# Optimization experiments

Hardware: AMD Instinct MI355X
Metric: run time of the kernel (lower is better)

The kernel has to match this reference:

```python
import jax, jax.numpy as jnp
import numpy as np

EPS = 1e-10
ENTROPY_COEF = 0.1
COLSUM_COEF = 1.0


def setup_inputs() -> dict:
    key = jax.random.key(0)
    k1, k2, k3 = jax.random.split(key, 3)
    H, T, B, S = 512, 50003, 32, 256
    colsum_threshold = 0.5
    return {
        "text_input": jax.random.randint(k1, (B, S), 0, T, dtype=jnp.int32),
        "init_logits": jnp.zeros((H,), dtype=jnp.float32),
        "transition_logits": jax.random.normal(k2, (H, H), dtype=jnp.float32) * 0.1,
        "emission_logits": jax.random.normal(k3, (H, T), dtype=jnp.float32) * 0.1,
        "colsum_threshold": colsum_threshold,
    }


def reference(text_input, init_logits, transition_logits, emission_logits, colsum_threshold):
    # softmax-normalized HMM parameters
    text_pi = jax.nn.softmax(init_logits, axis=0)              # [H]
    text_A = jax.nn.softmax(transition_logits, axis=1)         # [H,H]
    text_B = jax.nn.softmax(emission_logits, axis=1)           # [H,T]

    log_pi = jnp.log(text_pi + EPS)                            # [H]
    log_A = jnpp = jnp.log(text_A + EPS)                       # [H,H]
    log_B = jnp.log(text_B + EPS)                              # [H,T]

    # gather per-token emission log-probs: [B,S,H]
    log_B_obs = log_B.T[text_input]

    # t = 0
    log_alpha0 = log_pi[None, :] + log_B_obs[:, 0, :]          # [B,H]

    def step(log_alpha, obs_t):
        # logsumexp over source state i: [B,H(i),1] + [1,H(i),H(j)] -> [B,H(j)]
        trans = log_alpha[:, :, None] + log_A[None, :, :]
        new_alpha = jax.nn.logsumexp(trans, axis=1) + obs_t
        return new_alpha, None

    obs_rest = jnp.swapaxes(log_B_obs[:, 1:, :], 0, 1)         # [S-1,B,H]
    log_alpha_final, _ = jax.lax.scan(step, log_alpha0, obs_rest)

    log_likelihood = jax.nn.logsumexp(log_alpha_final, axis=1)  # [B]
    likelihood_loss = -jnp.mean(log_likelihood)

    transition_entropy = -jnp.sum(text_A * jnp.log(text_A + EPS), axis=1)
    transition_entropy_loss = jnp.mean(transition_entropy) * ENTROPY_COEF

    col_sums = jnp.sum(text_A, axis=0)
    colsum_reg = jnp.sum(jax.nn.relu(colsum_threshold - col_sums)) * COLSUM_COEF

    hmm_loss = likelihood_loss + transition_entropy_loss + colsum_reg
    return text_pi, text_A, text_B, hmm_loss
```

## Files before the change

kernel.cpp:

```cpp
#include <hip/hip_runtime.h>
#include <hip/hip_bf16.h>
#include <stdint.h>

#define HH 512
#define BB 32
#define SSEQ 256
#define TVOC 50003
#define EPSF 1e-10f
#define EMSCALE 96.0f
#define TOTLOG 2759.2459164008406f

typedef float f32x4 __attribute__((ext_vector_type(4)));
typedef int v8i __attribute__((ext_vector_type(8)));

__device__ __forceinline__ float wave_max(float v) {
#pragma unroll
  for (int off = 32; off; off >>= 1) v = fmaxf(v, __shfl_xor(v, off));
  return v;
}
__device__ __forceinline__ float wave_sum(float v) {
#pragma unroll
  for (int off = 32; off; off >>= 1) v += __shfl_xor(v, off);
  return v;
}

__global__ __launch_bounds__(512) void init_ws_kernel(float* ws) {
  if (threadIdx.x < 8) ws[threadIdx.x] = 0.0f;
  ws[8 + threadIdx.x] = 0.0f;
}

__global__ __launch_bounds__(512) void softmax_pi_kernel(
    const float* __restrict__ x, float* __restrict__ pi) {
  const int tid = threadIdx.x;
  const int wv = tid >> 6, ln = tid & 63;
  __shared__ float red[8];
  float v = x[tid];
  float m = wave_max(v);
  if (ln == 0) red[wv] = m;
  __syncthreads();
  float M = red[0];
#pragma unroll
  for (int i = 1; i < 8; ++i) M = fmaxf(M, red[i]);
  float e = __expf(v - M);
  float s = wave_sum(e);
  __syncthreads();
  if (ln == 0) red[wv] = s;
  __syncthreads();
  float S = 0.f;
#pragma unroll
  for (int i = 0; i < 8; ++i) S += red[i];
  pi[tid] = e / S;
}

__global__ __launch_bounds__(512) void softmaxA_kernel(
    const float* __restrict__ tl, float* __restrict__ outA,
    float* __restrict__ ws_ent) {
  const int r = blockIdx.x, tid = threadIdx.x;
  const int wv = tid >> 6, ln = tid & 63;
  __shared__ float red[8];
  float v = tl[(size_t)r * HH + tid];
  float m = wave_max(v);
  if (ln == 0) red[wv] = m;
  __syncthreads();
  float M = red[0];
#pragma unroll
  for (int i = 1; i < 8; ++i) M = fmaxf(M, red[i]);
  float e = __expf(v - M);
  float s = wave_sum(e);
  __syncthreads();
  if (ln == 0) red[wv] = s;
  __syncthreads();
  float S = 0.f;
#pragma unroll
  for (int i = 0; i < 8; ++i) S += red[i];
  float p = e / S;
  outA[(size_t)r * HH + tid] = p;
  float ent = -p * __logf(p + EPSF);
  ent = wave_sum(ent);
  __syncthreads();
  if (ln == 0) red[wv] = ent;
  __syncthreads();
  if (tid == 0) {
    float tot = 0.f;
#pragma unroll
    for (int i = 0; i < 8; ++i) tot += red[i];
    atomicAdd(ws_ent, tot);
  }
}

__global__ __launch_bounds__(512) void colsum_partial_kernel(
    const float* __restrict__ outA, float* __restrict__ col) {
  const int j = threadIdx.x;
  const int i0 = blockIdx.x * 64;
  float s = 0.f;
#pragma unroll 4
  for (int i = i0; i < i0 + 64; ++i) s += outA[(size_t)i * HH + j];
  atomicAdd(&col[j], s);
}

__global__ __launch_bounds__(1024) void softmaxB_gather_kernel(
    const float* __restrict__ el, float* __restrict__ outB,
    const int* __restrict__ tok, __hip_bfloat16* __restrict__ ems) {
  const int r = blockIdx.x, tid = threadIdx.x;
  const float* x = el + (size_t)r * TVOC;
  float* yo = outB + (size_t)r * TVOC;
  const int mis = (int)(((16u - ((unsigned)(uintptr_t)x & 15u)) & 15u) >> 2);
  const int body = (TVOC - mis) >> 2;
  const int tailoff = mis + body * 4;

  float m = -1e30f, s = 0.f;
  auto upd = [&m, &s](float v) {
    if (v > m) { s = s * __expf(m - v) + 1.f; m = v; }
    else       { s += __expf(v - m); }
  };
  if (tid < mis) upd(x[tid]);
  const float4* x4 = (const float4*)(x + mis);
  for (int i = tid; i < body; i += 1024) {
    float4 v = x4[i];
    upd(v.x); upd(v.y); upd(v.z); upd(v.w);
  }
  for (int i = tailoff + tid; i < TVOC; i += 1024) upd(x[i]);

#pragma unroll
  for (int off = 32; off; off >>= 1) {
    float om = __shfl_down(m, off), os = __shfl_down(s, off);
    float nm = fmaxf(m, om);
    s = s * __expf(m - nm) + os * __expf(om - nm);
    m = nm;
  }
  __shared__ float sm[16], ssv[16];
  __shared__ float bM, biZ;
  if ((tid & 63) == 0) { sm[tid >> 6] = m; ssv[tid >> 6] = s; }
  __syncthreads();
  if (tid == 0) {
    float M = sm[0], S = ssv[0];
#pragma unroll
    for (int w = 1; w < 16; ++w) {
      float nm = fmaxf(M, sm[w]);
      S = S * __expf(M - nm) + ssv[w] * __expf(sm[w] - nm);
      M = nm;
    }
    bM = M; biZ = 1.f / S;
  }
  __syncthreads();
  const float M = bM, iZ = biZ;
  if (tid < mis) yo[tid] = __expf(x[tid] - M) * iZ;
  float4* y4 = (float4*)(yo + mis);
  for (int i = tid; i < body; i += 1024) {
    float4 v = x4[i];
    float4 o;
    o.x = __expf(v.x - M) * iZ;
    o.y = __expf(v.y - M) * iZ;
    o.z = __expf(v.z - M) * iZ;
    o.w = __expf(v.w - M) * iZ;
    y4[i] = o;
  }
  for (int i = tailoff + tid; i < TVOC; i += 1024)
    yo[i] = __expf(x[i] - M) * iZ;

  const float gs = EMSCALE * iZ;
  for (int idx = tid; idx < BB * SSEQ; idx += 1024) {
    const int sq = idx >> 5, b = idx & 31;
    const int t = tok[b * SSEQ + sq];
    ems[((size_t)sq * HH + r) * BB + b] = __float2bfloat16(__expf(x[t] - M) * gs);
  }
}

__global__ __launch_bounds__(1024) void scan_kernel(
    const float* __restrict__ d_pi, const float* __restrict__ d_A,
    const __hip_bfloat16* __restrict__ ems, float* __restrict__ ws_negll) {
  const int h = blockIdx.x;
  const int tid = threadIdx.x;
  const int lane = tid & 63;
  const int wave = tid >> 6;
  const int l15 = lane & 15;
  const int quad = lane >> 4;

  __shared__ __align__(16) unsigned char alpha[2][16][528];
  __shared__ float wmax[16][17];
  __shared__ float wsum[16][17];
  __shared__ float ls[16];

  const unsigned short* emsu = (const unsigned short*)ems;

  v8i aF[2][4];
#pragma unroll
  for (int n = 0; n < 2; ++n) {
    const int jg = wave * 32 + n * 16 + l15;
#pragma unroll
    for (int c = 0; c < 4; ++c) {
#pragma unroll
      for (int g = 0; g < 8; ++g) {
        const int k0 = c * 128 + quad * 32 + g * 4;
        const float v0 = d_A[(size_t)(k0 + 0) * HH + jg] * 512.0f;
        const float v1 = d_A[(size_t)(k0 + 1) * HH + jg] * 512.0f;
        const float v2 = d_A[(size_t)(k0 + 2) * HH + jg] * 512.0f;
        const float v3 = d_A[(size_t)(k0 + 3) * HH + jg] * 512.0f;
        int wrd = 0;
        wrd = __builtin_amdgcn_cvt_pk_fp8_f32(v0, v1, wrd, false);
        wrd = __builtin_amdgcn_cvt_pk_fp8_f32(v2, v3, wrd, true);
        aF[n][c][g] = wrd;
      }
    }
  }

  {
    const int b = wave;
    const int j0 = lane * 8;
    float vals[8];
    float m = -1e30f;
#pragma unroll
    for (int u = 0; u < 8; ++u) {
      const float e = __bfloat162float(ems[(size_t)(j0 + u) * BB + h * 16 + b]);
      vals[u] = (d_pi[j0 + u] + EPSF) * e;
      m = fmaxf(m, vals[u]);
    }
    m = wave_max(m);
    if (lane == 0) ls[b] = __logf(m);
    const float r = 1.0f / m;
    int lo = 0, hi = 0;
    lo = __builtin_amdgcn_cvt_pk_fp8_f32(vals[0] * r, vals[1] * r, lo, false);
    lo = __builtin_amdgcn_cvt_pk_fp8_f32(vals[2] * r, vals[3] * r, lo, true);
    hi = __builtin_amdgcn_cvt_pk_fp8_f32(vals[4] * r, vals[5] * r, hi, false);
    hi = __builtin_amdgcn_cvt_pk_fp8_f32(vals[6] * r, vals[7] * r, hi, true);
    *(unsigned int*)&alpha[0][b][j0]     = (unsigned)lo;
    *(unsigned int*)&alpha[0][b][j0 + 4] = (unsigned)hi;
  }
  __syncthreads();

  unsigned short evr[2][4];
#pragma unroll
  for (int n = 0; n < 2; ++n)
#pragma unroll
    for (int rg = 0; rg < 4; ++rg) {
      const int j = wave * 32 + n * 16 + quad * 4 + rg;
      evr[n][rg] = emsu[((size_t)1 * HH + j) * BB + h * 16 + l15];
    }

#pragma unroll 1
  for (int t = 1; t < SSEQ; ++t) {
    const int cur = (t - 1) & 1, nxt = t & 1;

    float ev[2][4];
#pragma unroll
    for (int n = 0; n < 2; ++n)
#pragma unroll
      for (int rg = 0; rg < 4; ++rg) {
        const unsigned u = (unsigned)evr[n][rg] << 16;
        ev[n][rg] = __uint_as_float(u);
      }
    const int tp = (t + 1 < SSEQ) ? t + 1 : SSEQ - 1;
#pragma unroll
    for (int n = 0; n < 2; ++n)
#pragma unroll
      for (int rg = 0; rg < 4; ++rg) {
        const int j = wave * 32 + n * 16 + quad * 4 + rg;
        evr[n][rg] = emsu[((size_t)tp * HH + j) * BB + h * 16 + l15];
      }

    f32x4 acc0 = {0.f, 0.f, 0.f, 0.f}, acc1 = {0.f, 0.f, 0.f, 0.f};
#pragma unroll
    for (int c = 0; c < 4; ++c) {
      const unsigned char* ap = &alpha[cur][l15][c * 128 + quad * 32];
      const int4 lo = *(const int4*)ap;
      const int4 hi = *(const int4*)(ap + 16);
      v8i bf;
      bf[0] = lo.x; bf[1] = lo.y; bf[2] = lo.z; bf[3] = lo.w;
      bf[4] = hi.x; bf[5] = hi.y; bf[6] = hi.z; bf[7] = hi.w;
      acc0 = __builtin_amdgcn_mfma_scale_f32_16x16x128_f8f6f4(
          aF[0][c], bf, acc0, 0, 0, 0, 0x7F7F7F7F, 0, 0x7F7F7F7F);
      acc1 = __builtin_amdgcn_mfma_scale_f32_16x16x128_f8f6f4(
          aF[1][c], bf, acc1, 0, 0, 0, 0x7F7F7F7F, 0, 0x7F7F7F7F);
    }

    float y[2][4];
#pragma unroll
    for (int rg = 0; rg < 4; ++rg) {
      y[0][rg] = acc0[rg] * ev[0][rg];
      y[1][rg] = acc1[rg] * ev[1][rg];
    }

    float r = 1.0f;
    if ((t & 15) == 0) {
      float mm = -1e30f;
#pragma unroll
      for (int rg = 0; rg < 4; ++rg)
        mm = fmaxf(mm, fmaxf(y[0][rg], y[1][rg]));
      mm = fmaxf(mm, __shfl_xor(mm, 16));
      mm = fmaxf(mm, __shfl_xor(mm, 32));
      if (lane < 16) wmax[wave][lane] = mm;
      __syncthreads();
      float m = wmax[0][l15];
#pragma unroll
      for (int w = 1; w < 16; ++w) m = fmaxf(m, wmax[w][l15]);
      r = 1.0f / m;
      if (tid < 16) ls[tid] += __logf(m);
    }

#pragma unroll
    for (int n = 0; n < 2; ++n) {
      int d = 0;
      d = __builtin_amdgcn_cvt_pk_fp8_f32(y[n][0] * r, y[n][1] * r, d, false);
      d = __builtin_amdgcn_cvt_pk_fp8_f32(y[n][2] * r, y[n][3] * r, d, true);
      *(unsigned int*)&alpha[nxt][l15][wave * 32 + n * 16 + quad * 4] = (unsigned)d;
    }
    if (t == SSEQ - 1) {
      float s = (y[0][0] + y[0][1] + y[0][2] + y[0][3] +
                 y[1][0] + y[1][1] + y[1][2] + y[1][3]) * r;
      s += __shfl_xor(s, 16);
      s += __shfl_xor(s, 32);
      if (lane < 16) wsum[wave][lane] = s;
    }
    __syncthreads();
  }

  if (wave == 0 && lane < 16) {
    float s = 0.f;
#pragma unroll
    for (int w = 0; w < 16; ++w) s += wsum[w][lane];
    const float LL = __logf(s) + ls[lane] - TOTLOG;
    atomicAdd(ws_negll, -LL * (1.0f / 32.0f));
  }
}

__global__ __launch_bounds__(512) void finalize_kernel(
    const float* __restrict__ ws, const float* __restrict__ col,
    const float* __restrict__ thr, float* __restrict__ out_loss) {
  const int j = threadIdx.x;
  float v = fmaxf(thr[0] - col[j], 0.f);
  v = wave_sum(v);
  __shared__ float red[8];
  if ((j & 63) == 0) red[j >> 6] = v;
  __syncthreads();
  if (j == 0) {
    float creg = 0.f;
#pragma unroll
    for (int i = 0; i < 8; ++i) creg += red[i];
    out_loss[0] = ws[1] + ws[0] * (0.1f / 512.0f) + creg;
  }
}

extern "C" void kernel_launch(void* const* d_in, const int* in_sizes, int n_in,
                              void* d_out, int out_size, void* d_ws, size_t ws_size,
                              hipStream_t stream) {
  const int*   tok    = (const int*)d_in[0];
  const float* initl  = (const float*)d_in[1];
  const float* transl = (const float*)d_in[2];
  const float* eml    = (const float*)d_in[3];
  const float* thr    = (const float*)d_in[4];

  float* out      = (float*)d_out;
  float* out_pi   = out;
  float* out_A    = out + HH;
  float* out_B    = out + HH + (size_t)HH * HH;
  float* out_loss = out + HH + (size_t)HH * HH + (size_t)HH * TVOC;

  float* wsf = (float*)d_ws;
  float* col = wsf + 8;
  __hip_bfloat16* ems = (__hip_bfloat16*)((char*)d_ws + 4096);

  init_ws_kernel<<<1, 512, 0, stream>>>(wsf);
  softmax_pi_kernel<<<1, 512, 0, stream>>>(initl, out_pi);
  softmaxA_kernel<<<512, 512, 0, stream>>>(transl, out_A, wsf + 0);
  colsum_partial_kernel<<<8, 512, 0, stream>>>(out_A, col);
  softmaxB_gather_kernel<<<512, 1024, 0, stream>>>(eml, out_B, tok, ems);
  scan_kernel<<<2, 1024, 0, stream>>>(out_pi, out_A, ems, wsf + 1);
  finalize_kernel<<<1, 512, 0, stream>>>(wsf, col, thr, out_loss);
}
```

Baseline: 596.8 us.

## Halve scan block to 8 waves, repack emission layout for vector loads, split softmax accumulators

The scan kernel now runs 512 threads per block, with each wave computing 64 output states (four MFMA accumulators) instead of 32. This cuts the cost of the per-step block barrier and the cross-wave max reduction. The emission buffer is re-laid out so each lane fetches four consecutive states' bf16 values in one 8-byte load rather than four scalar loads. The loop is also unrolled by two. The softmaxB online max/sum now keeps four independent accumulator chains per thread to break the serial dependency, which costs extra registers and a final merge.

```diff
diff --git a/kernel.cpp b/kernel.cpp
--- a/kernel.cpp
+++ b/kernel.cpp
@@ -108,18 +108,26 @@
   const int body = (TVOC - mis) >> 2;
   const int tailoff = mis + body * 4;
 
-  float m = -1e30f, s = 0.f;
-  auto upd = [&m, &s](float v) {
+  float m0 = -1e30f, s0 = 0.f, m1 = -1e30f, s1 = 0.f;
+  float m2 = -1e30f, s2 = 0.f, m3 = -1e30f, s3 = 0.f;
+  auto upd = [](float& m, float& s, float v) {
     if (v > m) { s = s * __expf(m - v) + 1.f; m = v; }
     else       { s += __expf(v - m); }
   };
-  if (tid < mis) upd(x[tid]);
+  if (tid < mis) upd(m0, s0, x[tid]);
   const float4* x4 = (const float4*)(x + mis);
   for (int i = tid; i < body; i += 1024) {
     float4 v = x4[i];
-    upd(v.x); upd(v.y); upd(v.z); upd(v.w);
-  }
-  for (int i = tailoff + tid; i < TVOC; i += 1024) upd(x[i]);
+    upd(m0, s0, v.x); upd(m1, s1, v.y); upd(m2, s2, v.z); upd(m3, s3, v.w);
+  }
+  for (int i = tailoff + tid; i < TVOC; i += 1024) upd(m0, s0, x[i]);
+  auto mrg = [](float& m, float& s, float om, float os) {
+    float nm = fmaxf(m, om);
+    s = s * __expf(m - nm) + os * __expf(om - nm);
+    m = nm;
+  };
+  mrg(m0, s0, m1, s1); mrg(m2, s2, m3, s3); mrg(m0, s0, m2, s2);
+  float m = m0, s = s0;
 
 #pragma unroll
   for (int off = 32; off; off >>= 1) {
@@ -159,14 +167,16 @@
     yo[i] = __expf(x[i] - M) * iZ;
 
   const float gs = EMSCALE * iZ;
+  const int rg = r >> 2, rl = r & 3;
   for (int idx = tid; idx < BB * SSEQ; idx += 1024) {
     const int sq = idx >> 5, b = idx & 31;
     const int t = tok[b * SSEQ + sq];
-    ems[((size_t)sq * HH + r) * BB + b] = __float2bfloat16(__expf(x[t] - M) * gs);
-  }
-}
-
-__global__ __launch_bounds__(1024) void scan_kernel(
+    ems[((size_t)(sq * 128 + rg) * 32 + b) * 4 + rl] =
+        __float2bfloat16(__expf(x[t] - M) * gs);
+  }
+}
+
+__global__ __launch_bounds__(512, 2) void scan_kernel(
     const float* __restrict__ d_pi, const float* __restrict__ d_A,
     const __hip_bfloat16* __restrict__ ems, float* __restrict__ ws_negll) {
   const int h = blockIdx.x;
@@ -175,18 +185,20 @@
   const int wave = tid >> 6;
   const int l15 = lane & 15;
   const int quad = lane >> 4;
+  const int bG = h * 16 + l15;
 
   __shared__ __align__(16) unsigned char alpha[2][16][528];
-  __shared__ float wmax[16][17];
-  __shared__ float wsum[16][17];
+  __shared__ float wmax[8][17];
+  __shared__ float wsum[8][17];
   __shared__ float ls[16];
 
   const unsigned short* emsu = (const unsigned short*)ems;
-
-  v8i aF[2][4];
-#pragma unroll
-  for (int n = 0; n < 2; ++n) {
-    const int jg = wave * 32 + n * 16 + l15;
+  const uint2* emv = (const uint2*)ems;
+
+  v8i aF[4][4];
+#pragma unroll
+  for (int n = 0; n < 4; ++n) {
+    const int jg = wave * 64 + n * 16 + l15;
 #pragma unroll
     for (int c = 0; c < 4; ++c) {
 #pragma unroll
@@ -204,15 +216,18 @@
     }
   }
 
-  {
-    const int b = wave;
+#pragma unroll
+  for (int it = 0; it < 2; ++it) {
+    const int b = wave * 2 + it;
+    const int bb = h * 16 + b;
     const int j0 = lane * 8;
     float vals[8];
     float m = -1e30f;
 #pragma unroll
     for (int u = 0; u < 8; ++u) {
-      const float e = __bfloat162float(ems[(size_t)(j0 + u) * BB + h * 16 + b]);
-      vals[u] = (d_pi[j0 + u] + EPSF) * e;
+      const int j = j0 + u;
+      const unsigned ew = (unsigned)emsu[((size_t)(j >> 2) * 32 + bb) * 4 + (j & 3)] << 16;
+      vals[u] = (d_pi[j] + EPSF) * __uint_as_float(ew);
       m = fmaxf(m, vals[u]);
     }
     m = wave_max(m);
@@ -228,85 +243,85 @@
   }
   __syncthreads();
 
-  unsigned short evr[2][4];
-#pragma unroll
-  for (int n = 0; n < 2; ++n)
-#pragma unroll
-    for (int rg = 0; rg < 4; ++rg) {
-      const int j = wave * 32 + n * 16 + quad * 4 + rg;
-      evr[n][rg] = emsu[((size_t)1 * HH + j) * BB + h * 16 + l15];
-    }
-
-#pragma unroll 1
+  const uint2* ep = emv + ((size_t)1 * 128 + wave * 16 + quad) * 32 + bG;
+  uint2 evr[4];
+#pragma unroll
+  for (int n = 0; n < 4; ++n) evr[n] = ep[n * 128];
+  ep += 128 * 32;
+
+#pragma unroll 2
   for (int t = 1; t < SSEQ; ++t) {
     const int cur = (t - 1) & 1, nxt = t & 1;
 
-    float ev[2][4];
-#pragma unroll
-    for (int n = 0; n < 2; ++n)
-#pragma unroll
-      for (int rg = 0; rg < 4; ++rg) {
-        const unsigned u = (unsigned)evr[n][rg] << 16;
-        ev[n][rg] = __uint_as_float(u);
-      }
-    const int tp = (t + 1 < SSEQ) ? t + 1 : SSEQ - 1;
-#pragma unroll
-    for (int n = 0; n < 2; ++n)
-#pragma unroll
-      for (int rg = 0; rg < 4; ++rg) {
-        const int j = wave * 32 + n * 16 + quad * 4 + rg;
-        evr[n][rg] = emsu[((size_t)tp * HH + j) * BB + h * 16 + l15];
-      }
+    float ev[4][4];
+#pragma unroll
+    for (int n = 0; n < 4; ++n) {
+      ev[n][0] = __uint_as_float(evr[n].x << 16);
+      ev[n][1] = __uint_as_float(evr[n].x & 0xFFFF0000u);
+      ev[n][2] = __uint_as_float(evr[n].y << 16);
+      ev[n][3] = __uint_as_float(evr[n].y & 0xFFFF0000u);
+    }
+#pragma unroll
+    for (int n = 0; n < 4; ++n) evr[n] = ep[n * 128];
+    if (t <= SSEQ - 3) ep += 128 * 32;
 
     f32x4 acc0 = {0.f, 0.f, 0.f, 0.f}, acc1 = {0.f, 0.f, 0.f, 0.f};
+    f32x4 acc2 = {0.f, 0.f, 0.f, 0.f}, acc3 = {0.f, 0.f, 0.f, 0.f};
 #pragma unroll
     for (int c = 0; c < 4; ++c) {
       const unsigned char* ap = &alpha[cur][l15][c * 128 + quad * 32];
-      const int4 lo = *(const int4*)ap;
-      const int4 hi = *(const int4*)(ap + 16);
       v8i bf;
-      bf[0] = lo.x; bf[1] = lo.y; bf[2] = lo.z; bf[3] = lo.w;
-      bf[4] = hi.x; bf[5] = hi.y; bf[6] = hi.z; bf[7] = hi.w;
+      *(int4*)&bf       = *(const int4*)ap;
+      *(((int4*)&bf)+1) = *(const int4*)(ap + 16);
       acc0 = __builtin_amdgcn_mfma_scale_f32_16x16x128_f8f6f4(
           aF[0][c], bf, acc0, 0, 0, 0, 0x7F7F7F7F, 0, 0x7F7F7F7F);
       acc1 = __builtin_amdgcn_mfma_scale_f32_16x16x128_f8f6f4(
           aF[1][c], bf, acc1, 0, 0, 0, 0x7F7F7F7F, 0, 0x7F7F7F7F);
-    }
-
-    float y[2][4];
+      acc2 = __builtin_amdgcn_mfma_scale_f32_16x16x128_f8f6f4(
+          aF[2][c], bf, acc2, 0, 0, 0, 0x7F7F7F7F, 0, 0x7F7F7F7F);
+      acc3 = __builtin_amdgcn_mfma_scale_f32_16x16x128_f8f6f4(
+          aF[3][c], bf, acc3, 0, 0, 0, 0x7F7F7F7F, 0, 0x7F7F7F7F);
+    }
+
+    float y[4][4];
 #pragma unroll
     for (int rg = 0; rg < 4; ++rg) {
       y[0][rg] = acc0[rg] * ev[0][rg];
       y[1][rg] = acc1[rg] * ev[1][rg];
+      y[2][rg] = acc2[rg] * ev[2][rg];
+      y[3][rg] = acc3[rg] * ev[3][rg];
     }
 
     float r = 1.0f;
     if ((t & 15) == 0) {
       float mm = -1e30f;
 #pragma unroll
-      for (int rg = 0; rg < 4; ++rg)
-        mm = fmaxf(mm, fmaxf(y[0][rg], y[1][rg]));
+      for (int n = 0; n < 4; ++n)
+#pragma unroll
+        for (int rg = 0; rg < 4; ++rg) mm = fmaxf(mm, y[n][rg]);
       mm = fmaxf(mm, __shfl_xor(mm, 16));
       mm = fmaxf(mm, __shfl_xor(mm, 32));
       if (lane < 16) wmax[wave][lane] = mm;
       __syncthreads();
       float m = wmax[0][l15];
 #pragma unroll
-      for (int w = 1; w < 16; ++w) m = fmaxf(m, wmax[w][l15]);
+      for (int w = 1; w < 8; ++w) m = fmaxf(m, wmax[w][l15]);
       r = 1.0f / m;
       if (tid < 16) ls[tid] += __logf(m);
     }
 
 #pragma unroll
-    for (int n = 0; n < 2; ++n) {
+    for (int n = 0; n < 4; ++n) {
       int d = 0;
       d = __builtin_amdgcn_cvt_pk_fp8_f32(y[n][0] * r, y[n][1] * r, d, false);
       d = __builtin_amdgcn_cvt_pk_fp8_f32(y[n][2] * r, y[n][3] * r, d, true);
-      *(unsigned int*)&alpha[nxt][l15][wave * 32 + n * 16 + quad * 4] = (unsigned)d;
+      *(unsigned int*)&alpha[nxt][l15][wave * 64 + n * 16 + quad * 4] = (unsigned)d;
     }
     if (t == SSEQ - 1) {
-      float s = (y[0][0] + y[0][1] + y[0][2] + y[0][3] +
-                 y[1][0] + y[1][1] + y[1][2] + y[1][3]) * r;
+      float s = 0.f;
+#pragma unroll
+      for (int n = 0; n < 4; ++n) s += y[n][0] + y[n][1] + y[n][2] + y[n][3];
+      s *= r;
       s += __shfl_xor(s, 16);
       s += __shfl_xor(s, 32);
       if (lane < 16) wsum[wave][lane] = s;
@@ -317,7 +332,7 @@
   if (wave == 0 && lane < 16) {
     float s = 0.f;
 #pragma unroll
-    for (int w = 0; w < 16; ++w) s += wsum[w][lane];
+    for (int w = 0; w < 8; ++w) s += wsum[w][lane];
     const float LL = __logf(s) + ls[lane] - TOTLOG;
     atomicAdd(ws_negll, -LL * (1.0f / 32.0f));
   }
@@ -364,6 +379,6 @@
   softmaxA_kernel<<<512, 512, 0, stream>>>(transl, out_A, wsf + 0);
   colsum_partial_kernel<<<8, 512, 0, stream>>>(out_A, col);
   softmaxB_gather_kernel<<<512, 1024, 0, stream>>>(eml, out_B, tok, ems);
-  scan_kernel<<<2, 1024, 0, stream>>>(out_pi, out_A, ems, wsf + 1);
+  scan_kernel<<<2, 512, 0, stream>>>(out_pi, out_A, ems, wsf + 1);
   finalize_kernel<<<1, 512, 0, stream>>>(wsf, col, thr, out_loss);
 }
```

New measurement: 665.5 us. +11.5%, slower.
